# Kernel tuning notes

Measured on AMD Instinct MI355X. Metric: run time of the kernel, lower is better.

## Reference

```python
import jax, jax.numpy as jnp
import numpy as np

EPS_BN = 1e-5
EPS_W = 1e-8


def setup_inputs() -> dict:
    key = jax.random.key(0)
    ks = jax.random.split(key, 6)
    B, N, S, D1, D2 = 8, 8192, 2048, 128, 256
    Cin = D1 + D2  # 384
    return {
        "points_position": jax.random.normal(ks[0], (B, 3, N), jnp.float32),
        "sampled_points_position": jax.random.normal(ks[1], (B, 3, S), jnp.float32),
        "skip_points_feature": jax.random.normal(ks[2], (B, D1, N), jnp.float32),
        "sampled_points_feature": jax.random.normal(ks[3], (B, D2, S), jnp.float32),
        "W1": jax.random.normal(ks[4], (256, Cin), jnp.float32) * 0.05,
        "b1": jnp.zeros((256,), jnp.float32),
        "g1": jnp.ones((256,), jnp.float32),
        "beta1": jnp.zeros((256,), jnp.float32),
        "W2": jax.random.normal(ks[5], (128, 256), jnp.float32) * 0.05,
        "b2": jnp.zeros((128,), jnp.float32),
        "g2": jnp.ones((128,), jnp.float32),
        "beta2": jnp.zeros((128,), jnp.float32),
    }


def _bn_relu(x, g, b):
    # train-mode BatchNorm1d over (batch, points) per channel, x: [B,N,C]
    mean = jnp.mean(x, axis=(0, 1), keepdims=True)
    var = jnp.mean(jnp.square(x - mean), axis=(0, 1), keepdims=True)  # biased var
    return jax.nn.relu((x - mean) * jax.lax.rsqrt(var + EPS_BN) * g + b)


def reference(points_position, sampled_points_position, skip_points_feature,
              sampled_points_feature, W1, b1, g1, beta1, W2, b2, g2, beta2):
    pos = points_position.transpose(0, 2, 1)            # [B,N,3]
    spos = sampled_points_position.transpose(0, 2, 1)   # [B,S,3]
    sfeat = sampled_points_feature.transpose(0, 2, 1)   # [B,S,D2]

    # squared pairwise distance [B,N,S]
    d = (jnp.sum(pos * pos, axis=-1, keepdims=True)
         - 2.0 * jnp.einsum("bnc,bsc->bns", pos, spos)
         + jnp.sum(spos * spos, axis=-1)[:, None, :])

    # 3 nearest neighbors (smallest distances)
    neg_d3, idx = jax.lax.top_k(-d, 3)                  # [B,N,3]
    d3 = -neg_d3
    w = 1.0 / (d3 + EPS_W)
    w = w / jnp.sum(w, axis=-1, keepdims=True)          # [B,N,3]

    gathered = jax.vmap(lambda f, i: f[i])(sfeat, idx)  # [B,N,3,D2]
    interp = jnp.einsum("bnk,bnkd->bnd", w, gathered)   # [B,N,D2]

    feat = jnp.concatenate([skip_points_feature.transpose(0, 2, 1), interp], axis=-1)  # [B,N,D1+D2]

    h = _bn_relu(jnp.einsum("bnc,oc->bno", feat, W1) + b1, g1, beta1)  # [B,N,256]
    h = _bn_relu(jnp.einsum("bnc,oc->bno", h, W2) + b2, g2, beta2)     # [B,N,128]
    return h.transpose(0, 2, 1)                          # [B,128,N]
```

## Files before the change

### kernel.cpp

```cpp
#include <hip/hip_runtime.h>

constexpr int BATCH = 8;
constexpr int NPT   = 8192;
constexpr int NSMP  = 2048;
constexpr int D1C   = 128;
constexpr int D2C   = 256;
constexpr int CIN   = 384;
constexpr int C1    = 256;
constexpr int C2    = 128;
constexpr int BN_TOTAL = BATCH * NPT;

constexpr int BM = 128, BK = 32;
constexpr int NRB = BN_TOTAL / BM;

typedef __bf16 bf16x8 __attribute__((ext_vector_type(8)));
typedef short  s16x8  __attribute__((ext_vector_type(8)));
typedef float  f32x4  __attribute__((ext_vector_type(4)));
typedef unsigned short u16x4 __attribute__((ext_vector_type(4)));

__device__ __forceinline__ unsigned short f2bf(float x) {
  unsigned u = __builtin_bit_cast(unsigned, x);
  u += 0x7fffu + ((u >> 16) & 1u);
  return (unsigned short)(u >> 16);
}
__device__ __forceinline__ float bf2f(unsigned short h) {
  return __builtin_bit_cast(float, (unsigned)h << 16);
}

__device__ __forceinline__ void gld_lds16(const void* g, void* l) {
  __builtin_amdgcn_global_load_lds(
      (const __attribute__((address_space(1))) void*)g,
      (__attribute__((address_space(3))) void*)l, 16, 0, 0);
}

constexpr int PT_T = (NSMP / 32) * (D2C / 32) * BATCH;
constexpr int PT_S = (NPT / 32) * (D1C / 32) * BATCH;
constexpr int PT_M = (C1 * CIN + 255) / 256;

__global__ __launch_bounds__(256) void prep_all(
    const float* __restrict__ sfeat, float* __restrict__ sfeatT,
    const float* __restrict__ skip, unsigned short* __restrict__ featB,
    const float* __restrict__ spos, float* __restrict__ sposI,
    float4* __restrict__ qs4,
    const float* __restrict__ W1, unsigned short* __restrict__ W1h,
    const float* __restrict__ W2, unsigned short* __restrict__ W2h,
    float* __restrict__ stats) {
  __shared__ float tile[32][33];
  int bid = blockIdx.x, tid = threadIdx.x;
  int tx = tid & 31, ty = tid >> 5;
  if (bid < PT_T) {
    int z = bid >> 9;
    int r = bid & 511;
    int c0 = (r & 63) * 32;
    int r0 = (r >> 6) * 32;
    const float* inb = sfeat + (size_t)z * D2C * NSMP;
    float* outb = sfeatT + (size_t)z * NSMP * D2C;
#pragma unroll
    for (int i = 0; i < 32; i += 8)
      tile[ty + i][tx] = inb[(size_t)(r0 + ty + i) * NSMP + c0 + tx];
    __syncthreads();
#pragma unroll
    for (int i = 0; i < 32; i += 8)
      outb[(size_t)(c0 + ty + i) * D2C + r0 + tx] = tile[tx][ty + i];
  } else if (bid < PT_T + PT_S) {
    int id = bid - PT_T;
    int z = id >> 10;
    int r = id & 1023;
    int n0 = (r & 255) * 32;
    int d0 = (r >> 8) * 32;
#pragma unroll
    for (int i = 0; i < 32; i += 8)
      tile[ty + i][tx] = skip[((size_t)z * D1C + d0 + ty + i) * NPT + n0 + tx];
    __syncthreads();
#pragma unroll
    for (int i = 0; i < 32; i += 8) {
      int n = n0 + ty + i;
      featB[((size_t)z * NPT + n) * CIN + d0 + tx] = f2bf(tile[tx][ty + i]);
    }
  } else {
    int g = (bid - PT_T - PT_S) * 256 + tid;
    if (g < 768) stats[g] = 0.f;
    if (g < C1 * CIN) W1h[g] = f2bf(W1[g]);
    if (g < C2 * C1)  W2h[g] = f2bf(W2[g]);
    if (g < BATCH * NSMP) {
      int b = g >> 11, s = g & (NSMP - 1);
      const float* sp = spos + (size_t)b * 3 * NSMP;
      float x = sp[s], y = sp[NSMP + s], z = sp[2 * NSMP + s];
      sposI[(size_t)g * 3 + 0] = x;
      sposI[(size_t)g * 3 + 1] = y;
      sposI[(size_t)g * 3 + 2] = z;
      qs4[g] = make_float4(-2.f * x, -2.f * y, -2.f * z,
                           fmaf(x, x, fmaf(y, y, z * z)));
    }
  }
}

constexpr int KWAVES = 8;
constexpr int SEGK = NSMP / KWAVES;

__device__ __forceinline__ void ins_med3(float kf, float& k0, float& k1,
                                         float& k2, float& k3) {
  float o0 = k0, o1 = k1, o2 = k2;
  k0 = fminf(kf, o0);
  k1 = __builtin_amdgcn_fmed3f(kf, o0, o1);
  k2 = __builtin_amdgcn_fmed3f(kf, o1, o2);
  k3 = __builtin_amdgcn_fmed3f(kf, o2, k3);
}

__global__ __launch_bounds__(512, 2) void knn_scan(
    const float* __restrict__ pos,
    const float4* __restrict__ qs4g,
    float* __restrict__ mkG) {
  __shared__ __align__(16) float4 qs[NSMP];

  int tid = threadIdx.x;
  int wave = tid >> 6, lane = tid & 63;
  int blk = blockIdx.x;
  int b = blk & 7;
  int n0 = (blk >> 3) << 8;

  const float* pb = pos + (size_t)b * 3 * NPT;
  float px[4], py[4], pz[4], pp[4];
#pragma unroll
  for (int m = 0; m < 4; m++) {
    int n = n0 + (m << 6) + lane;
    px[m] = pb[n]; py[m] = pb[NPT + n]; pz[m] = pb[2 * NPT + n];
    pp[m] = fmaf(px[m], px[m], fmaf(py[m], py[m], pz[m] * pz[m]));
  }

  const float INF = __builtin_inff();
  float k0[4], k1[4], k2[4], k3[4];
#pragma unroll
  for (int m = 0; m < 4; m++) { k0[m] = INF; k1[m] = INF; k2[m] = INF; k3[m] = INF; }

  int s0 = wave * SEGK;
  const float4* qsrc = qs4g + (size_t)b * NSMP;
#pragma unroll
  for (int r = 0; r < 4; r++)
    gld_lds16(&qsrc[s0 + r * 64 + lane], &qs[s0 + r * 64]);
  __syncthreads();

#define KSTEP4(Q, SS)                                                        \
  {                                                                          \
    _Pragma("unroll")                                                        \
    for (int m_ = 0; m_ < 4; m_++) {                                         \
      float tt = (Q).w + pp[m_];       \
      float d_ = fmaf(px[m_], (Q).x,                                         \
                      fmaf(py[m_], (Q).y, fmaf(pz[m_], (Q).z, tt)));         \
      unsigned ki_ = (__builtin_bit_cast(unsigned, d_) & 0xFFFFF800u) |      \
                     (unsigned)(SS);                                         \
      ins_med3(__builtin_bit_cast(float, ki_), k0[m_], k1[m_], k2[m_], k3[m_]); \
    }                                                                        \
  }

  for (int t = 0; t < SEGK; t += 8) {
    float4 qv[8];
#pragma unroll
    for (int u = 0; u < 8; u++) qv[u] = qs[s0 + t + u];
#pragma unroll
    for (int u = 0; u < 8; u++) KSTEP4(qv[u], s0 + t + u)
  }
#undef KSTEP4

  size_t gbase = (size_t)b * NPT + n0 + lane;
#pragma unroll
  for (int m = 0; m < 4; m++) {
    size_t gp = gbase + (m << 6);
    mkG[(size_t)(wave * 4 + 0) * BN_TOTAL + gp] = k0[m];
    mkG[(size_t)(wave * 4 + 1) * BN_TOTAL + gp] = k1[m];
    mkG[(size_t)(wave * 4 + 2) * BN_TOTAL + gp] = k2[m];
    mkG[(size_t)(wave * 4 + 3) * BN_TOTAL + gp] = k3[m];
  }
}

__device__ __forceinline__ bool dless(double d, int i, double D, int I) {
  return d < D || (d == D && i < I);
}
__device__ __forceinline__ void dins3(double d, int i,
                                      double& b0, double& b1, double& b2,
                                      int& i0, int& i1, int& i2) {
  if (dless(d, i, b2, i2)) {
    if (dless(d, i, b1, i1)) {
      b2 = b1; i2 = i1;
      if (dless(d, i, b0, i0)) { b1 = b0; i1 = i0; b0 = d; i0 = i; }
      else                     { b1 = d; i1 = i; }
    } else { b2 = d; i2 = i; }
  }
}

constexpr int PPB_P = 64;

__global__ __launch_bounds__(256) void knn_post(
    const float* __restrict__ pos,
    const float* __restrict__ sposI,
    const float* __restrict__ mkG,
    const float* __restrict__ sfeatT,
    unsigned short* __restrict__ featB) {
  __shared__ int   il[PPB_P][3];
  __shared__ float wl[PPB_P][3];
  __shared__ int   fl[PPB_P];
  __shared__ int   fcnt;

  int tid = threadIdx.x;
  int wave = tid >> 6, lane = tid & 63;
  int blk = blockIdx.x;
  int b = blk & 7;
  int n0 = (blk >> 3) * PPB_P;

  if (tid == 0) fcnt = 0;
  __syncthreads();

  const float* pb = pos + (size_t)b * 3 * NPT;
  const float INF = __builtin_inff();

  if (tid < PPB_P) {
    size_t gp = (size_t)b * NPT + n0 + tid;
    float K0 = INF, K1 = INF, K2 = INF, K3 = INF;
#pragma unroll
    for (int pl = 0; pl < 32; pl++)
      ins_med3(mkG[(size_t)pl * BN_TOTAL + gp], K0, K1, K2, K3);

    int I0 = (int)(__builtin_bit_cast(unsigned, K0) & 0x7FFu);
    int I1 = (int)(__builtin_bit_cast(unsigned, K1) & 0x7FFu);
    int I2 = (int)(__builtin_bit_cast(unsigned, K2) & 0x7FFu);
    float d2m = __builtin_bit_cast(float, __builtin_bit_cast(unsigned, K2) & 0xFFFFF800u);
    float d3m = __builtin_bit_cast(float, __builtin_bit_cast(unsigned, K3) & 0xFFFFF800u);
    bool flag = (d3m - d2m) < 2e-3f * fmaxf(d3m, 0.f) + 1e-5f;
    if (flag) {
      int slot = atomicAdd(&fcnt, 1);
      fl[slot] = tid;
    }
    int n = n0 + tid;
    const float* q = sposI + (size_t)b * 3 * NSMP;
    double pxd = (double)pb[n], pyd = (double)pb[NPT + n], pzd = (double)pb[2 * NPT + n];
    double dd[3]; int II[3] = {I0, I1, I2};
#pragma unroll
    for (int k = 0; k < 3; k++) {
      double dx = pxd - (double)q[3 * II[k]];
      double dy = pyd - (double)q[3 * II[k] + 1];
      double dz = pzd - (double)q[3 * II[k] + 2];
      dd[k] = dx * dx + dy * dy + dz * dz;
    }
    double w0 = 1.0 / (dd[0] + 1e-8);
    double w1 = 1.0 / (dd[1] + 1e-8);
    double w2 = 1.0 / (dd[2] + 1e-8);
    double inv = 1.0 / (w0 + w1 + w2);
    il[tid][0] = I0; il[tid][1] = I1; il[tid][2] = I2;
    wl[tid][0] = (float)(w0 * inv);
    wl[tid][1] = (float)(w1 * inv);
    wl[tid][2] = (float)(w2 * inv);
  }
  __syncthreads();

  int fc = fcnt;
  for (int t = wave; t < fc; t += 4) {
    int P = fl[t];
    int n = n0 + P;
    double pxd = (double)pb[n], pyd = (double)pb[NPT + n], pzd = (double)pb[2 * NPT + n];
    const float* q = sposI + (size_t)b * 3 * NSMP;
    double b0 = 1e300, b1 = 1e300, b2 = 1e300;
    int i0 = 0x7FFFFFFF, i1 = 0x7FFFFFFF, i2 = 0x7FFFFFFF;
    for (int s = lane; s < NSMP; s += 64) {
      double dx = pxd - (double)q[3 * s];
      double dy = pyd - (double)q[3 * s + 1];
      double dz = pzd - (double)q[3 * s + 2];
      double d = dx * dx + dy * dy + dz * dz;
      dins3(d, s, b0, b1, b2, i0, i1, i2);
    }
#pragma unroll
    for (int m = 1; m < 64; m <<= 1) {
      double o0 = __shfl_xor(b0, m, 64), o1 = __shfl_xor(b1, m, 64), o2 = __shfl_xor(b2, m, 64);
      int    j0 = __shfl_xor(i0, m, 64), j1 = __shfl_xor(i1, m, 64), j2 = __shfl_xor(i2, m, 64);
      dins3(o0, j0, b0, b1, b2, i0, i1, i2);
      dins3(o1, j1, b0, b1, b2, i0, i1, i2);
      dins3(o2, j2, b0, b1, b2, i0, i1, i2);
    }
    if (lane == 0) {
      double w0 = 1.0 / (b0 + 1e-8);
      double w1 = 1.0 / (b1 + 1e-8);
      double w2 = 1.0 / (b2 + 1e-8);
      double inv = 1.0 / (w0 + w1 + w2);
      il[P][0] = i0; il[P][1] = i1; il[P][2] = i2;
      wl[P][0] = (float)(w0 * inv);
      wl[P][1] = (float)(w1 * inv);
      wl[P][2] = (float)(w2 * inv);
    }
  }
  __syncthreads();

  const float* base = sfeatT + (size_t)b * NSMP * D2C;
  for (int i = 0; i < 16; i++) {
    int P = (wave << 4) + i;
    int i0 = il[P][0], i1 = il[P][1], i2 = il[P][2];
    float w0 = wl[P][0], w1 = wl[P][1], w2 = wl[P][2];
    float4 v0 = *(const float4*)&base[(size_t)i0 * D2C + (lane << 2)];
    float4 v1 = *(const float4*)&base[(size_t)i1 * D2C + (lane << 2)];
    float4 v2 = *(const float4*)&base[(size_t)i2 * D2C + (lane << 2)];
    u16x4 o;
    o[0] = f2bf(w0 * v0.x + w1 * v1.x + w2 * v2.x);
    o[1] = f2bf(w0 * v0.y + w1 * v1.y + w2 * v2.y);
    o[2] = f2bf(w0 * v0.z + w1 * v1.z + w2 * v2.z);
    o[3] = f2bf(w0 * v0.w + w1 * v1.w + w2 * v2.w);
    *(u16x4*)&featB[((size_t)b * NPT + n0 + P) * CIN + D1C + (lane << 2)] = o;
  }
}

__global__ __launch_bounds__(256) void gemm1_mw(
    const unsigned short* __restrict__ featB,
    const unsigned short* __restrict__ W1h,
    const float* __restrict__ bias,
    unsigned short* __restrict__ Y1,
    float* __restrict__ sum1,
    float* __restrict__ sumsq1) {
  __shared__ __align__(16) unsigned short As[BM * BK];
  __shared__ __align__(16) unsigned short Bs[BM * BK];
  int tid = threadIdx.x;
  int lane = tid & 63, w = tid >> 6;
  int wr = w >> 1, wc = w & 1;
  int m16 = lane & 15, quad = lane >> 4;
  int cb = blockIdx.x, rb = blockIdx.y;
  int row0 = rb * BM, col0 = cb * BM;
  int srow = lane >> 2, scol8 = (lane & 3) * 8;

  f32x4 acc[4][4];
#pragma unroll
  for (int j = 0; j < 4; j++) {
    float bj = bias[col0 + wc * 64 + j * 16 + m16];
#pragma unroll
    for (int i = 0; i < 4; i++) acc[i][j] = f32x4{bj, bj, bj, bj};
  }

  for (int k0 = 0; k0 < CIN; k0 += BK) {
#pragma unroll
    for (int kq = 0; kq < 2; kq++) {
      int ar = 32 * w + 16 * kq + srow;
      int lb = __builtin_amdgcn_readfirstlane((32 * w + 16 * kq) * BK);
      gld_lds16(&featB[(size_t)(row0 + ar) * CIN + k0 + scol8], &As[lb]);
      gld_lds16(&W1h[(size_t)(col0 + ar) * CIN + k0 + scol8], &Bs[lb]);
    }
    __syncthreads();

    bf16x8 a[4], bb[4];
#pragma unroll
    for (int i = 0; i < 4; i++)
      a[i] = __builtin_bit_cast(bf16x8,
          *(const s16x8*)&As[(wr * 64 + i * 16 + m16) * BK + quad * 8]);
#pragma unroll
    for (int j = 0; j < 4; j++)
      bb[j] = __builtin_bit_cast(bf16x8,
          *(const s16x8*)&Bs[(wc * 64 + j * 16 + m16) * BK + quad * 8]);
#pragma unroll
    for (int i = 0; i < 4; i++)
#pragma unroll
      for (int j = 0; j < 4; j++)
        acc[i][j] = __builtin_amdgcn_mfma_f32_16x16x32_bf16(a[i], bb[j], acc[i][j], 0, 0, 0);
    __syncthreads();
  }

#pragma unroll
  for (int j = 0; j < 4; j++) {
    int col = col0 + wc * 64 + j * 16 + m16;
    float s = 0.f, q = 0.f;
#pragma unroll
    for (int i = 0; i < 4; i++)
#pragma unroll
      for (int r = 0; r < 4; r++) {
        float v = acc[i][j][r];
        Y1[(size_t)(row0 + wr * 64 + i * 16 + quad * 4 + r) * C1 + col] = f2bf(v);
        s += v; q = fmaf(v, v, q);
      }
    s += __shfl_xor(s, 16, 64); s += __shfl_xor(s, 32, 64);
    q += __shfl_xor(q, 16, 64); q += __shfl_xor(q, 32, 64);
    if (quad == 0) {
      atomicAdd(&sum1[col], s);
      atomicAdd(&sumsq1[col], q);
    }
  }
}

__global__ __launch_bounds__(256) void gemm2_mw(
    const unsigned short* __restrict__ Y1,
    const float* __restrict__ g1, const float* __restrict__ beta1,
    const float* __restrict__ sum1, const float* __restrict__ sumsq1,
    const unsigned short* __restrict__ W2h,
    const float* __restrict__ bias,
    unsigned short* __restrict__ Y2,
    float* __restrict__ sum2, float* __restrict__ sumsq2) {
  __shared__ __align__(16) unsigned short As[BM * BK];
  __shared__ __align__(16) unsigned short Bs[BM * BK];
  __shared__ float scs[C1], shs[C1];
  int tid = threadIdx.x;
  int lane = tid & 63, w = tid >> 6;
  int wr = w >> 1, wc = w & 1;
  int m16 = lane & 15, quad = lane >> 4;
  int rb = blockIdx.x;
  int row0 = rb * BM, col0 = 0;
  int srow = lane >> 2, scol8 = (lane & 3) * 8;

  {
    const float invBN = 1.0f / (float)BN_TOTAL;
    float mean = sum1[tid] * invBN;
    float var = sumsq1[tid] * invBN - mean * mean;
    float sc = g1[tid] / sqrtf(var + 1e-5f);
    scs[tid] = sc;
    shs[tid] = beta1[tid] - mean * sc;
  }

  f32x4 acc[4][4];
#pragma unroll
  for (int j = 0; j < 4; j++) {
    float bj = bias[col0 + wc * 64 + j * 16 + m16];
#pragma unroll
    for (int i = 0; i < 4; i++) acc[i][j] = f32x4{bj, bj, bj, bj};
  }
  __syncthreads();

  for (int k0 = 0; k0 < C1; k0 += BK) {
#pragma unroll
    for (int kq = 0; kq < 2; kq++) {
      int ar = 32 * w + 16 * kq + srow;
      int lb = __builtin_amdgcn_readfirstlane((32 * w + 16 * kq) * BK);
      gld_lds16(&W2h[(size_t)(col0 + ar) * C1 + k0 + scol8], &Bs[lb]);
      s16x8 v = *(const s16x8*)&Y1[(size_t)(row0 + ar) * C1 + k0 + scol8];
      unsigned short ov[8];
#pragma unroll
      for (int e = 0; e < 8; e++) {
        float x = bf2f((unsigned short)v[e]);
        float y = fmaxf(fmaf(x, scs[k0 + scol8 + e], shs[k0 + scol8 + e]), 0.f);
        ov[e] = f2bf(y);
      }
      *(s16x8*)&As[ar * BK + scol8] = *(const s16x8*)ov;
    }
    __syncthreads();

    bf16x8 a[4], bb[4];
#pragma unroll
    for (int i = 0; i < 4; i++)
      a[i] = __builtin_bit_cast(bf16x8,
          *(const s16x8*)&As[(wr * 64 + i * 16 + m16) * BK + quad * 8]);
#pragma unroll
    for (int j = 0; j < 4; j++)
      bb[j] = __builtin_bit_cast(bf16x8,
          *(const s16x8*)&Bs[(wc * 64 + j * 16 + m16) * BK + quad * 8]);
#pragma unroll
    for (int i = 0; i < 4; i++)
#pragma unroll
      for (int j = 0; j < 4; j++)
        acc[i][j] = __builtin_amdgcn_mfma_f32_16x16x32_bf16(a[i], bb[j], acc[i][j], 0, 0, 0);
    __syncthreads();
  }

#pragma unroll
  for (int j = 0; j < 4; j++) {
    int col = col0 + wc * 64 + j * 16 + m16;
    float s = 0.f, q = 0.f;
#pragma unroll
    for (int i = 0; i < 4; i++)
#pragma unroll
      for (int r = 0; r < 4; r++) {
        float v = acc[i][j][r];
        Y2[(size_t)(row0 + wr * 64 + i * 16 + quad * 4 + r) * C2 + col] = f2bf(v);
        s += v; q = fmaf(v, v, q);
      }
    s += __shfl_xor(s, 16, 64); s += __shfl_xor(s, 32, 64);
    q += __shfl_xor(q, 16, 64); q += __shfl_xor(q, 32, 64);
    if (quad == 0) {
      atomicAdd(&sum2[col], s);
      atomicAdd(&sumsq2[col], q);
    }
  }
}

__global__ void final_kernel(const unsigned short* __restrict__ Y2,
                             const float* __restrict__ sum2,
                             const float* __restrict__ sumsq2,
                             const float* __restrict__ g2,
                             const float* __restrict__ beta2,
                             float* __restrict__ out) {
  __shared__ float tile[32][33];
  int b = blockIdx.z;
  int n0 = blockIdx.x * 32;
  int c0 = blockIdx.y * 32;
  int tx = threadIdx.x, ty = threadIdx.y;
  int c = c0 + tx;
  const float invBN = 1.0f / (float)BN_TOTAL;
  float mean = sum2[c] * invBN;
  float var = sumsq2[c] * invBN - mean * mean;
  float sc = g2[c] / sqrtf(var + 1e-5f);
  float sh = beta2[c] - mean * sc;
#pragma unroll
  for (int i = 0; i < 32; i += 8) {
    int n = n0 + ty + i;
    float v = bf2f(Y2[((size_t)b * NPT + n) * C2 + c0 + tx]);
    tile[ty + i][tx] = fmaxf(fmaf(v, sc, sh), 0.f);
  }
  __syncthreads();
#pragma unroll
  for (int i = 0; i < 32; i += 8) {
    int cc = c0 + ty + i;
    out[((size_t)b * C2 + cc) * NPT + n0 + tx] = tile[tx][ty + i];
  }
}

extern "C" void kernel_launch(void* const* d_in, const int* in_sizes, int n_in,
                              void* d_out, int out_size, void* d_ws, size_t ws_size,
                              hipStream_t stream) {
  (void)in_sizes; (void)n_in; (void)out_size; (void)ws_size;
  const float* pos   = (const float*)d_in[0];
  const float* spos  = (const float*)d_in[1];
  const float* skip  = (const float*)d_in[2];
  const float* sfeat = (const float*)d_in[3];
  const float* W1    = (const float*)d_in[4];
  const float* b1    = (const float*)d_in[5];
  const float* g1    = (const float*)d_in[6];
  const float* beta1 = (const float*)d_in[7];
  const float* W2    = (const float*)d_in[8];
  const float* b2    = (const float*)d_in[9];
  const float* g2    = (const float*)d_in[10];
  const float* beta2 = (const float*)d_in[11];
  float* out = (float*)d_out;

  float* ws = (float*)d_ws;
  size_t off = 0;
  float* sfeatT  = ws + off; off += (size_t)BATCH * NSMP * D2C;
  unsigned short* featB = (unsigned short*)(ws + off); off += (size_t)BN_TOTAL * CIN / 2;
  unsigned short* Y1    = (unsigned short*)(ws + off); off += (size_t)BN_TOTAL * C1 / 2;
  unsigned short* Y2    = (unsigned short*)(ws + off); off += (size_t)BN_TOTAL * C2 / 2;
  unsigned short* W1h   = (unsigned short*)(ws + off); off += (size_t)C1 * CIN / 2;
  unsigned short* W2h   = (unsigned short*)(ws + off); off += (size_t)C2 * C1 / 2;
  float* sposI   = ws + off; off += (size_t)BATCH * NSMP * 3;
  float4* qs4    = (float4*)(ws + off); off += (size_t)BATCH * NSMP * 4;
  float* mkG     = ws + off; off += (size_t)32 * BN_TOTAL;
  float* stats   = ws + off; off += 1024;
  float* sum1   = stats;
  float* sumsq1 = stats + 256;
  float* sum2   = stats + 512;
  float* sumsq2 = stats + 640;

  prep_all<<<PT_T + PT_S + PT_M, 256, 0, stream>>>(
      sfeat, sfeatT, skip, featB, spos, sposI, qs4, W1, W1h, W2, W2h, stats);

  knn_scan<<<BN_TOTAL / 256, 512, 0, stream>>>(pos, qs4, mkG);

  knn_post<<<BN_TOTAL / PPB_P, 256, 0, stream>>>(pos, sposI, mkG, sfeatT, featB);

  gemm1_mw<<<dim3(C1 / BM, NRB), 256, 0, stream>>>(
      featB, W1h, b1, Y1, sum1, sumsq1);

  gemm2_mw<<<NRB, 256, 0, stream>>>(
      Y1, g1, beta1, sum1, sumsq1, W2h, b2, Y2, sum2, sumsq2);

  final_kernel<<<dim3(NPT / 32, C2 / 32, BATCH), dim3(32, 8), 0, stream>>>(
      Y2, sum2, sumsq2, g2, beta2, out);
}
```

Baseline: 303.5 us.

## Make knn_post wave-local with split merge; widen gemm1 to full output width

knn_post now gives each wave its own 16 points. Four lane groups each merge 8 of the 32 candidate planes, and the partial top-4 lists are combined with shuffles. Block-wide barriers and the shared atomic flag list are replaced by a per-wave ballot loop for the exact fallback search, and the feature gather is unrolled two points at a time. gemm1 now uses 512 threads per block covering all 256 output columns, so each feature row tile is loaded once instead of twice, at the cost of fewer, larger blocks.

```diff
diff --git a/kernel.cpp b/kernel.cpp
--- a/kernel.cpp
+++ b/kernel.cpp
@@ -188,7 +188,7 @@
   }
 }
 
-constexpr int PPB_P = 64;
+constexpr int PPW = 16;
 
 __global__ __launch_bounds__(256) void knn_post(
     const float* __restrict__ pos,
@@ -196,41 +196,56 @@
     const float* __restrict__ mkG,
     const float* __restrict__ sfeatT,
     unsigned short* __restrict__ featB) {
-  __shared__ int   il[PPB_P][3];
-  __shared__ float wl[PPB_P][3];
-  __shared__ int   fl[PPB_P];
-  __shared__ int   fcnt;
+  __shared__ int   il[4][PPW][3];
+  __shared__ float wl[4][PPW][3];
 
   int tid = threadIdx.x;
   int wave = tid >> 6, lane = tid & 63;
   int blk = blockIdx.x;
   int b = blk & 7;
-  int n0 = (blk >> 3) * PPB_P;
-
-  if (tid == 0) fcnt = 0;
-  __syncthreads();
+  int chunk = (blk >> 3) * 4 + wave;
+  int n0 = chunk * PPW;
+
+  int g  = lane >> 4;
+  int pt = lane & 15;
+  int n  = n0 + pt;
+  size_t gp = (size_t)b * NPT + n;
 
   const float* pb = pos + (size_t)b * 3 * NPT;
   const float INF = __builtin_inff();
 
-  if (tid < PPB_P) {
-    size_t gp = (size_t)b * NPT + n0 + tid;
-    float K0 = INF, K1 = INF, K2 = INF, K3 = INF;
-#pragma unroll
-    for (int pl = 0; pl < 32; pl++)
-      ins_med3(mkG[(size_t)pl * BN_TOTAL + gp], K0, K1, K2, K3);
-
-    int I0 = (int)(__builtin_bit_cast(unsigned, K0) & 0x7FFu);
-    int I1 = (int)(__builtin_bit_cast(unsigned, K1) & 0x7FFu);
-    int I2 = (int)(__builtin_bit_cast(unsigned, K2) & 0x7FFu);
-    float d2m = __builtin_bit_cast(float, __builtin_bit_cast(unsigned, K2) & 0xFFFFF800u);
-    float d3m = __builtin_bit_cast(float, __builtin_bit_cast(unsigned, K3) & 0xFFFFF800u);
-    bool flag = (d3m - d2m) < 2e-3f * fmaxf(d3m, 0.f) + 1e-5f;
-    if (flag) {
-      int slot = atomicAdd(&fcnt, 1);
-      fl[slot] = tid;
-    }
-    int n = n0 + tid;
+  float v0 = mkG[(size_t)(g * 8 + 0) * BN_TOTAL + gp];
+  float v1 = mkG[(size_t)(g * 8 + 1) * BN_TOTAL + gp];
+  float v2 = mkG[(size_t)(g * 8 + 2) * BN_TOTAL + gp];
+  float v3 = mkG[(size_t)(g * 8 + 3) * BN_TOTAL + gp];
+  float v4 = mkG[(size_t)(g * 8 + 4) * BN_TOTAL + gp];
+  float v5 = mkG[(size_t)(g * 8 + 5) * BN_TOTAL + gp];
+  float v6 = mkG[(size_t)(g * 8 + 6) * BN_TOTAL + gp];
+  float v7 = mkG[(size_t)(g * 8 + 7) * BN_TOTAL + gp];
+  float K0 = INF, K1 = INF, K2 = INF, K3 = INF;
+  ins_med3(v0, K0, K1, K2, K3); ins_med3(v1, K0, K1, K2, K3);
+  ins_med3(v2, K0, K1, K2, K3); ins_med3(v3, K0, K1, K2, K3);
+  ins_med3(v4, K0, K1, K2, K3); ins_med3(v5, K0, K1, K2, K3);
+  ins_med3(v6, K0, K1, K2, K3); ins_med3(v7, K0, K1, K2, K3);
+
+#pragma unroll
+  for (int mask = 16; mask <= 32; mask <<= 1) {
+    float o0 = __shfl_xor(K0, mask, 64);
+    float o1 = __shfl_xor(K1, mask, 64);
+    float o2 = __shfl_xor(K2, mask, 64);
+    float o3 = __shfl_xor(K3, mask, 64);
+    ins_med3(o0, K0, K1, K2, K3); ins_med3(o1, K0, K1, K2, K3);
+    ins_med3(o2, K0, K1, K2, K3); ins_med3(o3, K0, K1, K2, K3);
+  }
+
+  int I0 = (int)(__builtin_bit_cast(unsigned, K0) & 0x7FFu);
+  int I1 = (int)(__builtin_bit_cast(unsigned, K1) & 0x7FFu);
+  int I2 = (int)(__builtin_bit_cast(unsigned, K2) & 0x7FFu);
+  float d2m = __builtin_bit_cast(float, __builtin_bit_cast(unsigned, K2) & 0xFFFFF800u);
+  float d3m = __builtin_bit_cast(float, __builtin_bit_cast(unsigned, K3) & 0xFFFFF800u);
+  bool flag = (d3m - d2m) < 2e-3f * fmaxf(d3m, 0.f) + 1e-5f;
+
+  {
     const float* q = sposI + (size_t)b * 3 * NSMP;
     double pxd = (double)pb[n], pyd = (double)pb[NPT + n], pzd = (double)pb[2 * NPT + n];
     double dd[3]; int II[3] = {I0, I1, I2};
@@ -245,18 +260,20 @@
     double w1 = 1.0 / (dd[1] + 1e-8);
     double w2 = 1.0 / (dd[2] + 1e-8);
     double inv = 1.0 / (w0 + w1 + w2);
-    il[tid][0] = I0; il[tid][1] = I1; il[tid][2] = I2;
-    wl[tid][0] = (float)(w0 * inv);
-    wl[tid][1] = (float)(w1 * inv);
-    wl[tid][2] = (float)(w2 * inv);
-  }
-  __syncthreads();
-
-  int fc = fcnt;
-  for (int t = wave; t < fc; t += 4) {
-    int P = fl[t];
-    int n = n0 + P;
-    double pxd = (double)pb[n], pyd = (double)pb[NPT + n], pzd = (double)pb[2 * NPT + n];
+    if (g == 0) {
+      il[wave][pt][0] = I0; il[wave][pt][1] = I1; il[wave][pt][2] = I2;
+      wl[wave][pt][0] = (float)(w0 * inv);
+      wl[wave][pt][1] = (float)(w1 * inv);
+      wl[wave][pt][2] = (float)(w2 * inv);
+    }
+  }
+
+  unsigned long long fm = __ballot(flag) & 0xFFFFull;
+  while (fm) {
+    int P = __ffsll(fm) - 1;
+    fm &= fm - 1;
+    int nf = n0 + P;
+    double pxd = (double)pb[nf], pyd = (double)pb[NPT + nf], pzd = (double)pb[2 * NPT + nf];
     const float* q = sposI + (size_t)b * 3 * NSMP;
     double b0 = 1e300, b1 = 1e300, b2 = 1e300;
     int i0 = 0x7FFFFFFF, i1 = 0x7FFFFFFF, i2 = 0x7FFFFFFF;
@@ -280,32 +297,41 @@
       double w1 = 1.0 / (b1 + 1e-8);
       double w2 = 1.0 / (b2 + 1e-8);
       double inv = 1.0 / (w0 + w1 + w2);
-      il[P][0] = i0; il[P][1] = i1; il[P][2] = i2;
-      wl[P][0] = (float)(w0 * inv);
-      wl[P][1] = (float)(w1 * inv);
-      wl[P][2] = (float)(w2 * inv);
-    }
-  }
-  __syncthreads();
+      il[wave][P][0] = i0; il[wave][P][1] = i1; il[wave][P][2] = i2;
+      wl[wave][P][0] = (float)(w0 * inv);
+      wl[wave][P][1] = (float)(w1 * inv);
+      wl[wave][P][2] = (float)(w2 * inv);
+    }
+  }
 
   const float* base = sfeatT + (size_t)b * NSMP * D2C;
-  for (int i = 0; i < 16; i++) {
-    int P = (wave << 4) + i;
-    int i0 = il[P][0], i1 = il[P][1], i2 = il[P][2];
-    float w0 = wl[P][0], w1 = wl[P][1], w2 = wl[P][2];
-    float4 v0 = *(const float4*)&base[(size_t)i0 * D2C + (lane << 2)];
-    float4 v1 = *(const float4*)&base[(size_t)i1 * D2C + (lane << 2)];
-    float4 v2 = *(const float4*)&base[(size_t)i2 * D2C + (lane << 2)];
-    u16x4 o;
-    o[0] = f2bf(w0 * v0.x + w1 * v1.x + w2 * v2.x);
-    o[1] = f2bf(w0 * v0.y + w1 * v1.y + w2 * v2.y);
-    o[2] = f2bf(w0 * v0.z + w1 * v1.z + w2 * v2.z);
-    o[3] = f2bf(w0 * v0.w + w1 * v1.w + w2 * v2.w);
-    *(u16x4*)&featB[((size_t)b * NPT + n0 + P) * CIN + D1C + (lane << 2)] = o;
-  }
-}
-
-__global__ __launch_bounds__(256) void gemm1_mw(
+  for (int i = 0; i < PPW; i += 2) {
+    int P0 = i, P1 = i + 1;
+    int a0 = il[wave][P0][0], a1 = il[wave][P0][1], a2 = il[wave][P0][2];
+    int c0 = il[wave][P1][0], c1 = il[wave][P1][1], c2 = il[wave][P1][2];
+    float aw0 = wl[wave][P0][0], aw1 = wl[wave][P0][1], aw2 = wl[wave][P0][2];
+    float cw0 = wl[wave][P1][0], cw1 = wl[wave][P1][1], cw2 = wl[wave][P1][2];
+    float4 u0 = *(const float4*)&base[(size_t)a0 * D2C + (lane << 2)];
+    float4 u1 = *(const float4*)&base[(size_t)a1 * D2C + (lane << 2)];
+    float4 u2 = *(const float4*)&base[(size_t)a2 * D2C + (lane << 2)];
+    float4 v0f = *(const float4*)&base[(size_t)c0 * D2C + (lane << 2)];
+    float4 v1f = *(const float4*)&base[(size_t)c1 * D2C + (lane << 2)];
+    float4 v2f = *(const float4*)&base[(size_t)c2 * D2C + (lane << 2)];
+    u16x4 o0, o1;
+    o0[0] = f2bf(aw0 * u0.x + aw1 * u1.x + aw2 * u2.x);
+    o0[1] = f2bf(aw0 * u0.y + aw1 * u1.y + aw2 * u2.y);
+    o0[2] = f2bf(aw0 * u0.z + aw1 * u1.z + aw2 * u2.z);
+    o0[3] = f2bf(aw0 * u0.w + aw1 * u1.w + aw2 * u2.w);
+    o1[0] = f2bf(cw0 * v0f.x + cw1 * v1f.x + cw2 * v2f.x);
+    o1[1] = f2bf(cw0 * v0f.y + cw1 * v1f.y + cw2 * v2f.y);
+    o1[2] = f2bf(cw0 * v0f.z + cw1 * v1f.z + cw2 * v2f.z);
+    o1[3] = f2bf(cw0 * v0f.w + cw1 * v1f.w + cw2 * v2f.w);
+    *(u16x4*)&featB[((size_t)b * NPT + n0 + P0) * CIN + D1C + (lane << 2)] = o0;
+    *(u16x4*)&featB[((size_t)b * NPT + n0 + P1) * CIN + D1C + (lane << 2)] = o1;
+  }
+}
+
+__global__ __launch_bounds__(512) void gemm1_mw(
     const unsigned short* __restrict__ featB,
     const unsigned short* __restrict__ W1h,
     const float* __restrict__ bias,
@@ -313,30 +339,34 @@
     float* __restrict__ sum1,
     float* __restrict__ sumsq1) {
   __shared__ __align__(16) unsigned short As[BM * BK];
-  __shared__ __align__(16) unsigned short Bs[BM * BK];
+  __shared__ __align__(16) unsigned short Bs[C1 * BK];
   int tid = threadIdx.x;
   int lane = tid & 63, w = tid >> 6;
-  int wr = w >> 1, wc = w & 1;
+  int wr = w >> 2, wc = w & 3;
   int m16 = lane & 15, quad = lane >> 4;
-  int cb = blockIdx.x, rb = blockIdx.y;
-  int row0 = rb * BM, col0 = cb * BM;
+  int rb = blockIdx.x;
+  int row0 = rb * BM;
   int srow = lane >> 2, scol8 = (lane & 3) * 8;
 
   f32x4 acc[4][4];
 #pragma unroll
   for (int j = 0; j < 4; j++) {
-    float bj = bias[col0 + wc * 64 + j * 16 + m16];
+    float bj = bias[wc * 64 + j * 16 + m16];
 #pragma unroll
     for (int i = 0; i < 4; i++) acc[i][j] = f32x4{bj, bj, bj, bj};
   }
 
   for (int k0 = 0; k0 < CIN; k0 += BK) {
-#pragma unroll
-    for (int kq = 0; kq < 2; kq++) {
-      int ar = 32 * w + 16 * kq + srow;
-      int lb = __builtin_amdgcn_readfirstlane((32 * w + 16 * kq) * BK);
-      gld_lds16(&featB[(size_t)(row0 + ar) * CIN + k0 + scol8], &As[lb]);
-      gld_lds16(&W1h[(size_t)(col0 + ar) * CIN + k0 + scol8], &Bs[lb]);
+    {
+      int lb = __builtin_amdgcn_readfirstlane((w * 16) * BK);
+      gld_lds16(&featB[(size_t)(row0 + w * 16 + srow) * CIN + k0 + scol8],
+                &As[lb]);
+    }
+#pragma unroll
+    for (int rr = 0; rr < 2; rr++) {
+      int lb = __builtin_amdgcn_readfirstlane((rr * 128 + w * 16) * BK);
+      gld_lds16(&W1h[(size_t)(rr * 128 + w * 16 + srow) * CIN + k0 + scol8],
+                &Bs[lb]);
     }
     __syncthreads();
 
@@ -359,7 +389,7 @@
 
 #pragma unroll
   for (int j = 0; j < 4; j++) {
-    int col = col0 + wc * 64 + j * 16 + m16;
+    int col = wc * 64 + j * 16 + m16;
     float s = 0.f, q = 0.f;
 #pragma unroll
     for (int i = 0; i < 4; i++)
@@ -542,10 +572,9 @@
 
   knn_scan<<<BN_TOTAL / 256, 512, 0, stream>>>(pos, qs4, mkG);
 
-  knn_post<<<BN_TOTAL / PPB_P, 256, 0, stream>>>(pos, sposI, mkG, sfeatT, featB);
-
-  gemm1_mw<<<dim3(C1 / BM, NRB), 256, 0, stream>>>(
-      featB, W1h, b1, Y1, sum1, sumsq1);
+  knn_post<<<BN_TOTAL / (PPW * 4), 256, 0, stream>>>(pos, sposI, mkG, sfeatT, featB);
+
+  gemm1_mw<<<NRB, 512, 0, stream>>>(featB, W1h, b1, Y1, sum1, sumsq1);
 
   gemm2_mw<<<NRB, 256, 0, stream>>>(
       Y1, g1, beta1, sum1, sumsq1, W2h, b2, Y2, sum2, sumsq2);
```

After: 315.5 us. 1.04x slower.
